# Kernel optimization log

Measured on AMD Instinct MI355X. Metric: run time of the kernel, lower is better.

Reference implementation:

```python
import jax, jax.numpy as jnp
import numpy as np

K = 3  # deformable kernel size
OFFSET_CLIP = 10.0


def _conv2d_same(x, w, b):
    # 3x3 conv, stride 1, padding 1, NCHW/OIHW
    out = jax.lax.conv_general_dilated(
        x, w, window_strides=(1, 1), padding=((1, 1), (1, 1)),
        dimension_numbers=("NCHW", "OIHW", "NCHW"))
    return out + b[None, :, None, None]


def _deform_conv2d(x, offset, weight):
    """torchvision-style deform_conv2d, stride 1, pad 1, dilation 1, no bias.
    x:      [B, C, H, W]
    offset: [B, 2*K*K, H, W]  (per tap: dy then dx)
    weight: [Cout, C, K, K]
    """
    B, C, H, W = x.shape
    off = offset.reshape(B, K * K, 2, H, W)
    ky, kx = jnp.meshgrid(jnp.arange(K, dtype=x.dtype), jnp.arange(K, dtype=x.dtype), indexing="ij")
    ky = ky.reshape(-1)  # [9]
    kx = kx.reshape(-1)
    # sample coords: p0 - pad + k + offset  -> [B, 9, H, W]
    ys = jnp.arange(H, dtype=x.dtype)[None, None, :, None] - 1.0 + ky[None, :, None, None] + off[:, :, 0]
    xs = jnp.arange(W, dtype=x.dtype)[None, None, None, :] - 1.0 + kx[None, :, None, None] + off[:, :, 1]
    y0 = jnp.floor(ys)
    x0 = jnp.floor(xs)
    ty = ys - y0  # fractional parts, [B,9,H,W]
    tx = xs - x0
    iy0 = y0.astype(jnp.int32)
    ix0 = x0.astype(jnp.int32)

    xf = x.reshape(B, C, H * W)

    def gather(iy, ix):
        valid = ((iy >= 0) & (iy < H) & (ix >= 0) & (ix < W)).astype(x.dtype)
        idx = (jnp.clip(iy, 0, H - 1) * W + jnp.clip(ix, 0, W - 1)).reshape(B, -1)
        v = jax.vmap(lambda xv, iv: xv[:, iv])(xf, idx)  # [B, C, 9*H*W]
        return v.reshape(B, C, K * K, H, W) * valid[:, None]

    v00 = gather(iy0, ix0)
    v01 = gather(iy0, ix0 + 1)
    v10 = gather(iy0 + 1, ix0)
    v11 = gather(iy0 + 1, ix0 + 1)

    w00 = ((1.0 - ty) * (1.0 - tx))[:, None]  # [B,1,9,H,W]
    w01 = ((1.0 - ty) * tx)[:, None]
    w10 = (ty * (1.0 - tx))[:, None]
    w11 = (ty * tx)[:, None]

    sampled = v00 * w00 + v01 * w01 + v10 * w10 + v11 * w11  # [B,C,9,H,W]
    return jnp.einsum("bckhw,ock->bohw", sampled, weight.reshape(weight.shape[0], C, K * K))


def setup_inputs() -> dict:
    key = jax.random.key(0)
    k1, k2, k3, k4 = jax.random.split(key, 4)
    B, C, H, W = 4, 64, 128, 128
    x = jax.random.normal(k1, (B, C, H, W), dtype=jnp.float32)
    ref = jax.random.normal(k2, (B, C, H, W), dtype=jnp.float32)
    # offset_conv: in=2C, out=2*3*3=18. (Original zero-inits; we use small random
    # weights so the deformable sampling path is nontrivially exercised.)
    offset_w = jax.random.normal(k3, (2 * K * K, 2 * C, K, K), dtype=jnp.float32) * 0.01
    offset_b = jnp.zeros((2 * K * K,), dtype=jnp.float32)
    # main deform weight: kaiming_normal fan_out, relu -> std = sqrt(2 / (Cout*K*K))
    std = float(np.sqrt(2.0 / (C * K * K)))
    weight = jax.random.normal(k4, (C, C, K, K), dtype=jnp.float32) * std
    return {"x": x, "ref": ref, "offset_w": offset_w, "offset_b": offset_b, "weight": weight}


def reference(x, ref, offset_w, offset_b, weight):
    combined = jnp.concatenate([x, ref], axis=1)
    offset = _conv2d_same(combined, offset_w, offset_b)
    offset = jnp.clip(offset, -OFFSET_CLIP, OFFSET_CLIP)
    aligned = _deform_conv2d(x, offset, weight)
    return aligned.astype(x.dtype)
```

## Files before the change

### kernel.cpp

```cpp
#include <hip/hip_runtime.h>

#define Bsz 4
#define Cch 64
#define Hh 128
#define Ww 128
#define NOFF 18
#define CK 576
#define CKPAD 580

typedef __attribute__((ext_vector_type(8))) short short8;
typedef __attribute__((ext_vector_type(4))) float floatx4;

__device__ __forceinline__ unsigned short f2bf(float f) {
    union { float f; unsigned u; } v; v.f = f;
    unsigned r = v.u + 0x7fff + ((v.u >> 16) & 1);
    return (unsigned short)(r >> 16);
}
__device__ __forceinline__ float bflo(unsigned d) {
    union { unsigned u; float f; } v; v.u = d << 16; return v.f;
}
__device__ __forceinline__ float bfhi(unsigned d) {
    union { unsigned u; float f; } v; v.u = d & 0xffff0000u; return v.f;
}
__device__ __forceinline__ unsigned cvtpk(float lo, float hi) {
    unsigned r;
    asm("v_cvt_pk_bf16_f32 %0, %1, %2" : "=v"(r) : "v"(lo), "v"(hi));
    return r;
}
__device__ __forceinline__ uint4 gld4(const void* p) {
    uint4 q;
    asm volatile("global_load_dwordx4 %0, %1, off" : "=v"(q) : "v"(p) : "memory");
    return q;
}

__global__ __launch_bounds__(256) void prep(const float* __restrict__ x,
                                            const float* __restrict__ ref,
                                            const float* __restrict__ wo,
                                            const float* __restrict__ w,
                                            unsigned* __restrict__ xpair,
                                            unsigned short* __restrict__ w9,
                                            unsigned short* __restrict__ wbf) {
    __shared__ unsigned tile[64][130];
    int bid = blockIdx.x;
    int tid = threadIdx.x;
    if (bid < 512) {
        int b = bid >> 7;
        int h = bid & 127;
        int px2 = tid & 63;
        int cg = tid >> 6;
        const float* xb = x + ((size_t)b << 20) + (h << 7) + (px2 << 1);
        const float* rb = ref + ((size_t)b << 20) + (h << 7) + (px2 << 1);
#pragma unroll
        for (int j = 0; j < 16; ++j) {
            int c0 = cg * 32 + 2 * j;
            const float* s = (c0 < 64) ? xb : rb;
            int cl = c0 & 63;
            float2 va = *(const float2*)(s + ((size_t)cl << 14));
            float2 vb = *(const float2*)(s + ((size_t)(cl + 1) << 14));
            unsigned w0 = (unsigned)f2bf(va.x) | ((unsigned)f2bf(vb.x) << 16);
            unsigned w1 = (unsigned)f2bf(va.y) | ((unsigned)f2bf(vb.y) << 16);
            *(uint2*)(&tile[c0 >> 1][px2 << 1]) = make_uint2(w0, w1);
        }
        __syncthreads();
#pragma unroll
        for (int it = 0; it < 16; ++it) {
            int idx = it * 256 + tid;
            int cq5 = idx & 31;
            int pos = idx >> 5;
            int posn = min(pos + 1, 127);
            unsigned t0 = tile[2 * cq5][pos], t0n = tile[2 * cq5][posn];
            unsigned t1 = tile[2 * cq5 + 1][pos], t1n = tile[2 * cq5 + 1][posn];
            uint4 o;
            o.x = (t0 & 0xffffu) | (t0n << 16);
            o.y = (t0 >> 16) | (t0n & 0xffff0000u);
            o.z = (t1 & 0xffffu) | (t1n << 16);
            o.w = (t1 >> 16) | (t1n & 0xffff0000u);
            *(uint4*)(xpair + (((size_t)(b << 14) + (h << 7) + pos) << 7) + (cq5 << 2)) = o;
        }
    } else if (bid < 656) {
        int t = (bid - 512) * 256 + tid;
        if (t < Cch * CK) {
            int oc = t / CK;
            int rem = t % CK;
            int k = rem >> 6, c = rem & 63;
            wbf[t] = f2bf(w[(oc * Cch + c) * 9 + k]);
        }
    } else {
        int t = (bid - 656) * 256 + tid;
        if (t < 9 * 32 * 128) {
            int ci = t & 127, ocp = (t >> 7) & 31, tap = t >> 12;
            w9[t] = (ocp < NOFF) ? f2bf(wo[(ocp * 128 + ci) * 9 + tap]) : (unsigned short)0;
        }
    }
}

__global__ __launch_bounds__(256, 3) void fused_align(
        const unsigned* __restrict__ xpair,
        const unsigned short* __restrict__ w9,
        const unsigned short* __restrict__ wbf,
        const float* __restrict__ bias,
        float* __restrict__ out) {
    __shared__ union {
        unsigned short tile3[3 * 34 * 128];
        unsigned short smp[32][CKPAD];
    } u;
    __shared__ float red[2][2][64][4];
    __shared__ float4 wts[288];
    __shared__ int2 meta[288];

    int bi0 = blockIdx.x;
    int bi = ((bi0 & 7) << 8) | (bi0 >> 3);
    int b = bi >> 9;
    int rem = bi & 511;
    int h = rem >> 2;
    int w0 = (rem & 3) << 5;
    int tid = threadIdx.x;
    int wv = tid >> 6, lane = tid & 63;
    int to = wv & 1;
    int kh = wv >> 1;
    int r16 = lane & 15;
    int g = lane >> 4;

    const unsigned* xp32 = xpair + ((size_t)b << 21);

    float bias4[4] = {0.f, 0.f, 0.f, 0.f};
    if (kh == 0) {
#pragma unroll
        for (int r = 0; r < 4; ++r) {
            int oc = to * 16 + g * 4 + r;
            if (oc < NOFF) bias4[r] = bias[oc];
        }
    }

    {
        uint4 qa[13];
        bool val[13];
#pragma unroll
        for (int it = 0; it < 13; ++it) {
            int idx = it * 256 + tid;
            int idc = (idx < 3264) ? idx : 0;
            int cq4 = idc & 31;
            int pos = idc >> 5;
            int row = pos / 34, xx = pos % 34;
            int yy = h + row - 1, xg = w0 + xx - 1;
            bool v = ((unsigned)yy < (unsigned)Hh) && ((unsigned)xg < (unsigned)Ww);
            val[it] = v;
            const unsigned* ap = xp32 + (((yy << 7) + xg) << 7) + (cq4 << 2);
            qa[it] = gld4(v ? (const void*)ap : (const void*)xp32);
        }
        asm volatile("s_waitcnt vmcnt(0)" ::: "memory");
        __builtin_amdgcn_sched_barrier(0);
#pragma unroll
        for (int it = 0; it < 13; ++it) {
            int idx = it * 256 + tid;
            if (idx < 3264) {
                int cq4 = idx & 31;
                int pos = idx >> 5;
                int xx = pos % 34;
                uint4 q = val[it] ? qa[it] : make_uint4(0u, 0u, 0u, 0u);
                unsigned p0v = (q.x & 0xffffu) | (q.y << 16);
                unsigned p1v = (q.z & 0xffffu) | (q.w << 16);
                int ci0 = cq4 << 2;
                *(uint2*)(&u.tile3[(pos << 7) + (ci0 ^ ((xx & 7) << 3))]) =
                    make_uint2(p0v, p1v);
            }
        }
    }
    __syncthreads();

    floatx4 accA0 = {0.f, 0.f, 0.f, 0.f};
    floatx4 accA1 = {0.f, 0.f, 0.f, 0.f};
#pragma unroll
    for (int tap = 0; tap < 9; ++tap) {
        int dy = tap / 3, dx = tap % 3;
        const unsigned short* arow = w9 + ((size_t)(tap * 32 + to * 16 + r16) << 7) + kh * 64;
        short8 a0 = *(const short8*)(arow + g * 8);
        short8 a1 = *(const short8*)(arow + 32 + g * 8);
#pragma unroll
        for (int s = 0; s < 2; ++s) {
            int xxr = r16 + dx + s * 16;
            const unsigned short* brow = &u.tile3[(dy * 34 + xxr) << 7];
            int sw = (xxr & 7) << 3;
            int cb0 = kh * 64 + g * 8;
            short8 bb0 = *(const short8*)(brow + (cb0 ^ sw));
            short8 bb1 = *(const short8*)(brow + ((cb0 + 32) ^ sw));
            if (s == 0) {
                accA0 = __builtin_amdgcn_mfma_f32_16x16x32_bf16(a0, bb0, accA0, 0, 0, 0);
                accA0 = __builtin_amdgcn_mfma_f32_16x16x32_bf16(a1, bb1, accA0, 0, 0, 0);
            } else {
                accA1 = __builtin_amdgcn_mfma_f32_16x16x32_bf16(a0, bb0, accA1, 0, 0, 0);
                accA1 = __builtin_amdgcn_mfma_f32_16x16x32_bf16(a1, bb1, accA1, 0, 0, 0);
            }
        }
    }
    if (kh == 1) {
#pragma unroll
        for (int r = 0; r < 4; ++r) { red[0][to][lane][r] = accA0[r]; red[1][to][lane][r] = accA1[r]; }
    }
    __syncthreads();

    if (kh == 0 && (to == 0 || g == 0)) {
        int ntap = (to == 0) ? 2 : 1;
        int kbase = (to * 16 + g * 4) >> 1;
#pragma unroll
        for (int s = 0; s < 2; ++s) {
            float vout[4];
#pragma unroll
            for (int r = 0; r < 4; ++r) {
                float v = (s == 0 ? accA0[r] : accA1[r]) + red[s][to][lane][r] + bias4[r];
                vout[r] = fminf(fmaxf(v, -10.0f), 10.0f);
            }
            int p = s * 16 + r16;
#pragma unroll
            for (int t = 0; t < 2; ++t) {
                if (t < ntap) {
                    int k = kbase + t;
                    float dyo = vout[2 * t], dxo = vout[2 * t + 1];
                    int ky = k / 3, kx = k % 3;
                    float ys = (float)(h - 1 + ky) + dyo;
                    float xs = (float)(w0 + p - 1 + kx) + dxo;
                    float fy = floorf(ys), fx = floorf(xs);
                    int iy0 = (int)fy, ix0 = (int)fx;
                    float ty = ys - fy, tx = xs - fx;
                    float wy0 = (1.f - ty) * (((unsigned)iy0 < (unsigned)Hh) ? 1.f : 0.f);
                    float wy1 = ty         * (((unsigned)(iy0 + 1) < (unsigned)Hh) ? 1.f : 0.f);
                    float wx0 = (1.f - tx) * (((unsigned)ix0 < (unsigned)Ww) ? 1.f : 0.f);
                    float wx1 = tx         * (((unsigned)(ix0 + 1) < (unsigned)Ww) ? 1.f : 0.f);
                    int ixb  = min(max(ix0, 0), Ww - 2);
                    int iy0c = min(max(iy0, 0), Hh - 1);
                    int iy1c = min(max(iy0 + 1, 0), Hh - 1);
                    bool s0v = (min(max(ix0, 0), Ww - 1) != ixb);
                    bool s1v = (min(max(ix0 + 1, 0), Ww - 1) != ixb);
                    float w00 = wy0 * wx0, w01 = wy0 * wx1, w10 = wy1 * wx0, w11 = wy1 * wx1;
                    float A  = (s0v ? 0.f : w00) + (s1v ? 0.f : w01);
                    float Bw = (s0v ? w00 : 0.f) + (s1v ? w01 : 0.f);
                    float Cw = (s0v ? 0.f : w10) + (s1v ? 0.f : w11);
                    float Dw = (s0v ? w10 : 0.f) + (s1v ? w11 : 0.f);
                    wts[p * 9 + k] = make_float4(A, Bw, Cw, Dw);
                    meta[p * 9 + k] = make_int2(((iy0c << 7) + ixb) << 9,
                                                ((iy1c << 7) + ixb) << 9);
                }
            }
        }
    }
    __syncthreads();

    {
        int p0 = tid >> 4, cq = tid & 15;
        const char* xbB = (const char*)xpair + ((size_t)b << 23) + cq * 16;
#pragma unroll
        for (int s = 0; s < 2; ++s) {
            int p = p0 + s * 16;
            uint4 q0[9], q1[9];
            float4 wt[9];
#pragma unroll
            for (int k = 0; k < 9; ++k) {
                int2 mm = meta[p * 9 + k];
                wt[k] = wts[p * 9 + k];
                q0[k] = gld4(xbB + mm.x);
                q1[k] = gld4(xbB + mm.y);
            }
            asm volatile("s_waitcnt vmcnt(0)" ::: "memory");
            __builtin_amdgcn_sched_barrier(0);
#pragma unroll
            for (int k = 0; k < 9; ++k) {
                uint4 qa = q0[k], qb = q1[k];
                float4 w = wt[k];
                float s0 = bflo(qa.x)*w.x + bfhi(qa.x)*w.y + bflo(qb.x)*w.z + bfhi(qb.x)*w.w;
                float s1 = bflo(qa.y)*w.x + bfhi(qa.y)*w.y + bflo(qb.y)*w.z + bfhi(qb.y)*w.w;
                float s2 = bflo(qa.z)*w.x + bfhi(qa.z)*w.y + bflo(qb.z)*w.z + bfhi(qb.z)*w.w;
                float s3 = bflo(qa.w)*w.x + bfhi(qa.w)*w.y + bflo(qb.w)*w.z + bfhi(qb.w)*w.w;
                *(uint2*)(&u.smp[p][k * 64 + cq * 4]) =
                    make_uint2(cvtpk(s0, s1), cvtpk(s2, s3));
            }
        }
    }
    __syncthreads();

    {
        floatx4 acc0 = {0.f, 0.f, 0.f, 0.f};
        floatx4 acc1 = {0.f, 0.f, 0.f, 0.f};
        const short8* ap = (const short8*)(wbf + (size_t)(wv * 16 + r16) * CK + g * 8);
        const unsigned short* bb0 = &u.smp[r16][g * 8];
        const unsigned short* bb1 = &u.smp[16 + r16][g * 8];
#pragma unroll
        for (int kk = 0; kk < 18; ++kk) {
            short8 a = ap[kk * 4];
            short8 v0 = *(const short8*)(bb0 + kk * 32);
            short8 v1 = *(const short8*)(bb1 + kk * 32);
            acc0 = __builtin_amdgcn_mfma_f32_16x16x32_bf16(a, v0, acc0, 0, 0, 0);
            acc1 = __builtin_amdgcn_mfma_f32_16x16x32_bf16(a, v1, acc1, 0, 0, 0);
        }
        size_t obase = ((size_t)(b * Cch + wv * 16 + g * 4)) << 14;
        int hw = (h << 7) + w0 + r16;
#pragma unroll
        for (int r = 0; r < 4; ++r) {
            out[obase + ((size_t)r << 14) + hw] = acc0[r];
            out[obase + ((size_t)r << 14) + hw + 16] = acc1[r];
        }
    }
}

extern "C" void kernel_launch(void* const* d_in, const int* in_sizes, int n_in,
                              void* d_out, int out_size, void* d_ws, size_t ws_size,
                              hipStream_t stream) {
    const float* x      = (const float*)d_in[0];
    const float* ref    = (const float*)d_in[1];
    const float* wo     = (const float*)d_in[2];
    const float* bias   = (const float*)d_in[3];
    const float* weight = (const float*)d_in[4];
    float* out = (float*)d_out;

    unsigned short* w9  = (unsigned short*)d_ws;
    unsigned short* wbf = (unsigned short*)((char*)d_ws + 262144);
    unsigned* xpair     = (unsigned*)((char*)d_ws + 524288);

    hipLaunchKernelGGL(prep, dim3(800), dim3(256), 0, stream,
                       x, ref, wo, weight, xpair, w9, wbf);
    hipLaunchKernelGGL(fused_align, dim3(2048), dim3(256), 0, stream,
                       xpair, w9, wbf, bias, out);
}
```

Measured before the change: 75.87 us.

## Overlap second-half gathers with first-half MFMA in deform conv

Splits the 32-pixel tile into two 16-pixel halves. It issues the bilinear gather loads for the second half before running the MFMA and output stores of the first half, so global gather latency overlaps with matrix compute. In exchange it adds a barrier, reloads the weight fragments for each half, and keeps 18 extra vector registers live across the MFMA loop, which may reduce occupancy.

```diff
diff --git a/kernel.cpp b/kernel.cpp
--- a/kernel.cpp
+++ b/kernel.cpp
@@ -248,56 +248,82 @@
     {
         int p0 = tid >> 4, cq = tid & 15;
         const char* xbB = (const char*)xpair + ((size_t)b << 23) + cq * 16;
-#pragma unroll
-        for (int s = 0; s < 2; ++s) {
-            int p = p0 + s * 16;
+        int p1 = p0 + 16;
+
+#define PACK9(p, qq0, qq1)                                                            \
+        _Pragma("unroll")                                                             \
+        for (int k = 0; k < 9; ++k) {                                                 \
+            float4 w = wts[(p) * 9 + k];                                              \
+            uint4 qa = qq0[k], qb = qq1[k];                                           \
+            float s0 = bflo(qa.x)*w.x + bfhi(qa.x)*w.y + bflo(qb.x)*w.z + bfhi(qb.x)*w.w; \
+            float s1 = bflo(qa.y)*w.x + bfhi(qa.y)*w.y + bflo(qb.y)*w.z + bfhi(qb.y)*w.w; \
+            float s2 = bflo(qa.z)*w.x + bfhi(qa.z)*w.y + bflo(qb.z)*w.z + bfhi(qb.z)*w.w; \
+            float s3 = bflo(qa.w)*w.x + bfhi(qa.w)*w.y + bflo(qb.w)*w.z + bfhi(qb.w)*w.w; \
+            *(uint2*)(&u.smp[p][k * 64 + cq * 4]) =                                   \
+                make_uint2(cvtpk(s0, s1), cvtpk(s2, s3));                             \
+        }
+
+        {
             uint4 q0[9], q1[9];
-            float4 wt[9];
 #pragma unroll
             for (int k = 0; k < 9; ++k) {
-                int2 mm = meta[p * 9 + k];
-                wt[k] = wts[p * 9 + k];
+                int2 mm = meta[p0 * 9 + k];
                 q0[k] = gld4(xbB + mm.x);
                 q1[k] = gld4(xbB + mm.y);
             }
             asm volatile("s_waitcnt vmcnt(0)" ::: "memory");
             __builtin_amdgcn_sched_barrier(0);
-#pragma unroll
-            for (int k = 0; k < 9; ++k) {
-                uint4 qa = q0[k], qb = q1[k];
-                float4 w = wt[k];
-                float s0 = bflo(qa.x)*w.x + bfhi(qa.x)*w.y + bflo(qb.x)*w.z + bfhi(qb.x)*w.w;
-                float s1 = bflo(qa.y)*w.x + bfhi(qa.y)*w.y + bflo(qb.y)*w.z + bfhi(qb.y)*w.w;
-                float s2 = bflo(qa.z)*w.x + bfhi(qa.z)*w.y + bflo(qb.z)*w.z + bfhi(qb.z)*w.w;
-                float s3 = bflo(qa.w)*w.x + bfhi(qa.w)*w.y + bflo(qb.w)*w.z + bfhi(qb.w)*w.w;
-                *(uint2*)(&u.smp[p][k * 64 + cq * 4]) =
-                    make_uint2(cvtpk(s0, s1), cvtpk(s2, s3));
-            }
-        }
-    }
-    __syncthreads();
-
-    {
-        floatx4 acc0 = {0.f, 0.f, 0.f, 0.f};
-        floatx4 acc1 = {0.f, 0.f, 0.f, 0.f};
-        const short8* ap = (const short8*)(wbf + (size_t)(wv * 16 + r16) * CK + g * 8);
-        const unsigned short* bb0 = &u.smp[r16][g * 8];
-        const unsigned short* bb1 = &u.smp[16 + r16][g * 8];
-#pragma unroll
-        for (int kk = 0; kk < 18; ++kk) {
-            short8 a = ap[kk * 4];
-            short8 v0 = *(const short8*)(bb0 + kk * 32);
-            short8 v1 = *(const short8*)(bb1 + kk * 32);
-            acc0 = __builtin_amdgcn_mfma_f32_16x16x32_bf16(a, v0, acc0, 0, 0, 0);
-            acc1 = __builtin_amdgcn_mfma_f32_16x16x32_bf16(a, v1, acc1, 0, 0, 0);
-        }
-        size_t obase = ((size_t)(b * Cch + wv * 16 + g * 4)) << 14;
-        int hw = (h << 7) + w0 + r16;
-#pragma unroll
-        for (int r = 0; r < 4; ++r) {
-            out[obase + ((size_t)r << 14) + hw] = acc0[r];
-            out[obase + ((size_t)r << 14) + hw + 16] = acc1[r];
-        }
+            PACK9(p0, q0, q1)
+        }
+
+        uint4 r0[9], r1[9];
+#pragma unroll
+        for (int k = 0; k < 9; ++k) {
+            int2 mm = meta[p1 * 9 + k];
+            r0[k] = gld4(xbB + mm.x);
+            r1[k] = gld4(xbB + mm.y);
+        }
+        __syncthreads();
+
+        {
+            floatx4 acc0 = {0.f, 0.f, 0.f, 0.f};
+            const short8* ap = (const short8*)(wbf + (size_t)(wv * 16 + r16) * CK + g * 8);
+            const unsigned short* bb0 = &u.smp[r16][g * 8];
+#pragma unroll
+            for (int kk = 0; kk < 18; ++kk) {
+                short8 a = ap[kk * 4];
+                short8 v0 = *(const short8*)(bb0 + kk * 32);
+                acc0 = __builtin_amdgcn_mfma_f32_16x16x32_bf16(a, v0, acc0, 0, 0, 0);
+            }
+            size_t obase = ((size_t)(b * Cch + wv * 16 + g * 4)) << 14;
+            int hw = (h << 7) + w0 + r16;
+#pragma unroll
+            for (int r = 0; r < 4; ++r)
+                out[obase + ((size_t)r << 14) + hw] = acc0[r];
+        }
+
+        asm volatile("s_waitcnt vmcnt(0)" ::: "memory");
+        __builtin_amdgcn_sched_barrier(0);
+        PACK9(p1, r0, r1)
+        __syncthreads();
+
+        {
+            floatx4 acc1 = {0.f, 0.f, 0.f, 0.f};
+            const short8* ap = (const short8*)(wbf + (size_t)(wv * 16 + r16) * CK + g * 8);
+            const unsigned short* bb1 = &u.smp[16 + r16][g * 8];
+#pragma unroll
+            for (int kk = 0; kk < 18; ++kk) {
+                short8 a = ap[kk * 4];
+                short8 v1 = *(const short8*)(bb1 + kk * 32);
+                acc1 = __builtin_amdgcn_mfma_f32_16x16x32_bf16(a, v1, acc1, 0, 0, 0);
+            }
+            size_t obase = ((size_t)(b * Cch + wv * 16 + g * 4)) << 14;
+            int hw = (h << 7) + w0 + r16 + 16;
+#pragma unroll
+            for (int r = 0; r < 4; ++r)
+                out[obase + ((size_t)r << 14) + hw] = acc1[r];
+        }
+#undef PACK9
     }
 }
 
```

Result: slower. 82.13 us (+8.3%).

## Shrink LDS footprint to fit four blocks per CU via union overlap

Applied to the files above, without the earlier changes.

Moves the reduction buffer, sampling weights and metadata into the same LDS union as the sampled tile, stores bilinear weights as packed fp16 instead of float4, and replaces the padded sampled-matrix layout with an XOR-swizzled unpadded one. Because the metadata now overlaps the sample buffer, the second pixel pass first copies its metadata into registers and adds extra barriers before overwriting. The aim is to cut LDS per block so launch bounds can request four blocks per CU, hiding gather latency with more waves. It risks register pressure under the tighter bound, extra syncs, and fp16 rounding of the interpolation weights.

```diff
diff --git a/kernel.cpp b/kernel.cpp
--- a/kernel.cpp
+++ b/kernel.cpp
@@ -6,10 +6,11 @@
 #define Ww 128
 #define NOFF 18
 #define CK 576
-#define CKPAD 580
+#define SMPB 1152
 
 typedef __attribute__((ext_vector_type(8))) short short8;
 typedef __attribute__((ext_vector_type(4))) float floatx4;
+typedef __fp16 half2v __attribute__((ext_vector_type(2)));
 
 __device__ __forceinline__ unsigned short f2bf(float f) {
     union { float f; unsigned u; } v; v.f = f;
@@ -27,10 +28,19 @@
     asm("v_cvt_pk_bf16_f32 %0, %1, %2" : "=v"(r) : "v"(lo), "v"(hi));
     return r;
 }
+__device__ __forceinline__ unsigned h2bits(half2v h) {
+    union { half2v h; unsigned u; } v; v.h = h; return v.u;
+}
+__device__ __forceinline__ half2v bits2h(unsigned u) {
+    union { half2v h; unsigned u; } v; v.u = u; return v.h;
+}
 __device__ __forceinline__ uint4 gld4(const void* p) {
     uint4 q;
     asm volatile("global_load_dwordx4 %0, %1, off" : "=v"(q) : "v"(p) : "memory");
     return q;
+}
+__device__ __forceinline__ char* smpp(char* base, int row, int bir) {
+    return base + row * SMPB + (bir ^ ((row & 7) << 4));
 }
 
 __global__ __launch_bounds__(256) void prep(const float* __restrict__ x,
@@ -94,19 +104,21 @@
     }
 }
 
-__global__ __launch_bounds__(256, 3) void fused_align(
+__global__ __launch_bounds__(256, 4) void fused_align(
         const unsigned* __restrict__ xpair,
         const unsigned short* __restrict__ w9,
         const unsigned short* __restrict__ wbf,
         const float* __restrict__ bias,
         float* __restrict__ out) {
     __shared__ union {
-        unsigned short tile3[3 * 34 * 128];
-        unsigned short smp[32][CKPAD];
+        struct {
+            unsigned short tile3[3 * 34 * 128];
+            float red[2][2][64][4];
+            uint2 wtsH[288];
+            int2 metaB[288];
+        } A;
+        unsigned short smp[32][576];
     } u;
-    __shared__ float red[2][2][64][4];
-    __shared__ float4 wts[288];
-    __shared__ int2 meta[288];
 
     int bi0 = blockIdx.x;
     int bi = ((bi0 & 7) << 8) | (bi0 >> 3);
@@ -161,7 +173,7 @@
                 unsigned p0v = (q.x & 0xffffu) | (q.y << 16);
                 unsigned p1v = (q.z & 0xffffu) | (q.w << 16);
                 int ci0 = cq4 << 2;
-                *(uint2*)(&u.tile3[(pos << 7) + (ci0 ^ ((xx & 7) << 3))]) =
+                *(uint2*)(&u.A.tile3[(pos << 7) + (ci0 ^ ((xx & 7) << 3))]) =
                     make_uint2(p0v, p1v);
             }
         }
@@ -179,7 +191,7 @@
 #pragma unroll
         for (int s = 0; s < 2; ++s) {
             int xxr = r16 + dx + s * 16;
-            const unsigned short* brow = &u.tile3[(dy * 34 + xxr) << 7];
+            const unsigned short* brow = &u.A.tile3[(dy * 34 + xxr) << 7];
             int sw = (xxr & 7) << 3;
             int cb0 = kh * 64 + g * 8;
             short8 bb0 = *(const short8*)(brow + (cb0 ^ sw));
@@ -195,7 +207,7 @@
     }
     if (kh == 1) {
 #pragma unroll
-        for (int r = 0; r < 4; ++r) { red[0][to][lane][r] = accA0[r]; red[1][to][lane][r] = accA1[r]; }
+        for (int r = 0; r < 4; ++r) { u.A.red[0][to][lane][r] = accA0[r]; u.A.red[1][to][lane][r] = accA1[r]; }
     }
     __syncthreads();
 
@@ -207,7 +219,7 @@
             float vout[4];
 #pragma unroll
             for (int r = 0; r < 4; ++r) {
-                float v = (s == 0 ? accA0[r] : accA1[r]) + red[s][to][lane][r] + bias4[r];
+                float v = (s == 0 ? accA0[r] : accA1[r]) + u.A.red[s][to][lane][r] + bias4[r];
                 vout[r] = fminf(fmaxf(v, -10.0f), 10.0f);
             }
             int p = s * 16 + r16;
@@ -236,9 +248,11 @@
                     float Bw = (s0v ? w00 : 0.f) + (s1v ? w01 : 0.f);
                     float Cw = (s0v ? 0.f : w10) + (s1v ? 0.f : w11);
                     float Dw = (s0v ? w10 : 0.f) + (s1v ? w11 : 0.f);
-                    wts[p * 9 + k] = make_float4(A, Bw, Cw, Dw);
-                    meta[p * 9 + k] = make_int2(((iy0c << 7) + ixb) << 9,
-                                                ((iy1c << 7) + ixb) << 9);
+                    u.A.wtsH[p * 9 + k] = make_uint2(
+                        h2bits(__builtin_amdgcn_cvt_pkrtz(A, Bw)),
+                        h2bits(__builtin_amdgcn_cvt_pkrtz(Cw, Dw)));
+                    u.A.metaB[p * 9 + k] = make_int2(((iy0c << 7) + ixb) << 9,
+                                                     ((iy1c << 7) + ixb) << 9);
                 }
             }
         }
@@ -248,15 +262,26 @@
     {
         int p0 = tid >> 4, cq = tid & 15;
         const char* xbB = (const char*)xpair + ((size_t)b << 23) + cq * 16;
-#pragma unroll
-        for (int s = 0; s < 2; ++s) {
-            int p = p0 + s * 16;
+        char* smpBase = (char*)u.smp;
+
+#define PACK1(p, qa, qb, whx, why)                                                    \
+        {                                                                             \
+            half2v hAB = bits2h(whx), hCD = bits2h(why);                              \
+            float wAv = (float)hAB.x, wBv = (float)hAB.y;                             \
+            float wCv = (float)hCD.x, wDv = (float)hCD.y;                             \
+            float s0 = bflo(qa.x)*wAv + bfhi(qa.x)*wBv + bflo(qb.x)*wCv + bfhi(qb.x)*wDv; \
+            float s1 = bflo(qa.y)*wAv + bfhi(qa.y)*wBv + bflo(qb.y)*wCv + bfhi(qb.y)*wDv; \
+            float s2 = bflo(qa.z)*wAv + bfhi(qa.z)*wBv + bflo(qb.z)*wCv + bfhi(qb.z)*wDv; \
+            float s3 = bflo(qa.w)*wAv + bfhi(qa.w)*wBv + bflo(qb.w)*wCv + bfhi(qb.w)*wDv; \
+            *(uint2*)smpp(smpBase, p, k * 128 + cq * 8) =                             \
+                make_uint2(cvtpk(s0, s1), cvtpk(s2, s3));                             \
+        }
+
+        {
             uint4 q0[9], q1[9];
-            float4 wt[9];
-#pragma unroll
-            for (int k = 0; k < 9; ++k) {
-                int2 mm = meta[p * 9 + k];
-                wt[k] = wts[p * 9 + k];
+#pragma unroll
+            for (int k = 0; k < 9; ++k) {
+                int2 mm = u.A.metaB[p0 * 9 + k];
                 q0[k] = gld4(xbB + mm.x);
                 q1[k] = gld4(xbB + mm.y);
             }
@@ -265,29 +290,50 @@
 #pragma unroll
             for (int k = 0; k < 9; ++k) {
                 uint4 qa = q0[k], qb = q1[k];
-                float4 w = wt[k];
-                float s0 = bflo(qa.x)*w.x + bfhi(qa.x)*w.y + bflo(qb.x)*w.z + bfhi(qb.x)*w.w;
-                float s1 = bflo(qa.y)*w.x + bfhi(qa.y)*w.y + bflo(qb.y)*w.z + bfhi(qb.y)*w.w;
-                float s2 = bflo(qa.z)*w.x + bfhi(qa.z)*w.y + bflo(qb.z)*w.z + bfhi(qb.z)*w.w;
-                float s3 = bflo(qa.w)*w.x + bfhi(qa.w)*w.y + bflo(qb.w)*w.z + bfhi(qb.w)*w.w;
-                *(uint2*)(&u.smp[p][k * 64 + cq * 4]) =
-                    make_uint2(cvtpk(s0, s1), cvtpk(s2, s3));
-            }
-        }
+                uint2 wh = u.A.wtsH[p0 * 9 + k];
+                PACK1(p0, qa, qb, wh.x, wh.y)
+            }
+        }
+        __syncthreads();
+
+        {
+            int p1 = p0 + 16;
+            int2 mreg[9];
+            uint2 wreg[9];
+#pragma unroll
+            for (int k = 0; k < 9; ++k) {
+                mreg[k] = u.A.metaB[p1 * 9 + k];
+                wreg[k] = u.A.wtsH[p1 * 9 + k];
+            }
+            __syncthreads();
+            uint4 q0[9], q1[9];
+#pragma unroll
+            for (int k = 0; k < 9; ++k) {
+                q0[k] = gld4(xbB + mreg[k].x);
+                q1[k] = gld4(xbB + mreg[k].y);
+            }
+            asm volatile("s_waitcnt vmcnt(0)" ::: "memory");
+            __builtin_amdgcn_sched_barrier(0);
+#pragma unroll
+            for (int k = 0; k < 9; ++k) {
+                uint4 qa = q0[k], qb = q1[k];
+                PACK1(p1, qa, qb, wreg[k].x, wreg[k].y)
+            }
+        }
+#undef PACK1
     }
     __syncthreads();
 
     {
+        char* smpBase = (char*)u.smp;
         floatx4 acc0 = {0.f, 0.f, 0.f, 0.f};
         floatx4 acc1 = {0.f, 0.f, 0.f, 0.f};
         const short8* ap = (const short8*)(wbf + (size_t)(wv * 16 + r16) * CK + g * 8);
-        const unsigned short* bb0 = &u.smp[r16][g * 8];
-        const unsigned short* bb1 = &u.smp[16 + r16][g * 8];
 #pragma unroll
         for (int kk = 0; kk < 18; ++kk) {
             short8 a = ap[kk * 4];
-            short8 v0 = *(const short8*)(bb0 + kk * 32);
-            short8 v1 = *(const short8*)(bb1 + kk * 32);
+            short8 v0 = *(const short8*)smpp(smpBase, r16, g * 16 + kk * 64);
+            short8 v1 = *(const short8*)smpp(smpBase, 16 + r16, g * 16 + kk * 64);
             acc0 = __builtin_amdgcn_mfma_f32_16x16x32_bf16(a, v0, acc0, 0, 0, 0);
             acc1 = __builtin_amdgcn_mfma_f32_16x16x32_bf16(a, v1, acc1, 0, 0, 0);
         }
```

Measured after the change: 66.63 us (median of 2 runs). -12.2%, faster.

## Shrink LDS footprint to raise occupancy: union buffers, fp16 weights, half-size sample tile

Applied to the files above, without the earlier changes.

Moves the reduction buffer into the shared union with the input tile, stores bilinear weights as packed fp16, and halves the sampled tile to 16 pixels. Sampling and the MFMA GEMM now alternate per 16-pixel half, with an XOR swizzle on the sample buffer. This cuts LDS use so the launch bound can rise from 3 to 5 blocks per SIMD, aiming to hide gather latency. In exchange it adds extra barriers, serialises the two halves, and loses some precision from fp16 weights.

```diff
diff --git a/kernel.cpp b/kernel.cpp
--- a/kernel.cpp
+++ b/kernel.cpp
@@ -6,10 +6,11 @@
 #define Ww 128
 #define NOFF 18
 #define CK 576
-#define CKPAD 580
+#define SMPB 1152
 
 typedef __attribute__((ext_vector_type(8))) short short8;
 typedef __attribute__((ext_vector_type(4))) float floatx4;
+typedef __fp16 half2v __attribute__((ext_vector_type(2)));
 
 __device__ __forceinline__ unsigned short f2bf(float f) {
     union { float f; unsigned u; } v; v.f = f;
@@ -27,10 +28,19 @@
     asm("v_cvt_pk_bf16_f32 %0, %1, %2" : "=v"(r) : "v"(lo), "v"(hi));
     return r;
 }
+__device__ __forceinline__ unsigned h2bits(half2v h) {
+    union { half2v h; unsigned u; } v; v.h = h; return v.u;
+}
+__device__ __forceinline__ half2v bits2h(unsigned u) {
+    union { half2v h; unsigned u; } v; v.u = u; return v.h;
+}
 __device__ __forceinline__ uint4 gld4(const void* p) {
     uint4 q;
     asm volatile("global_load_dwordx4 %0, %1, off" : "=v"(q) : "v"(p) : "memory");
     return q;
+}
+__device__ __forceinline__ char* smpp(char* base, int row, int bir) {
+    return base + row * SMPB + (bir ^ ((row & 7) << 4));
 }
 
 __global__ __launch_bounds__(256) void prep(const float* __restrict__ x,
@@ -94,19 +104,23 @@
     }
 }
 
-__global__ __launch_bounds__(256, 3) void fused_align(
+__global__ __launch_bounds__(256, 5) void fused_align(
         const unsigned* __restrict__ xpair,
         const unsigned short* __restrict__ w9,
         const unsigned short* __restrict__ wbf,
         const float* __restrict__ bias,
         float* __restrict__ out) {
     __shared__ union {
-        unsigned short tile3[3 * 34 * 128];
-        unsigned short smp[32][CKPAD];
+        struct {
+            unsigned short tile3[3 * 34 * 128];
+            float red[2][2][64][4];
+        } A;
+        struct {
+            uint2 wtsH[288];
+            int2 metaB[288];
+            unsigned short smp[16][576];
+        } B;
     } u;
-    __shared__ float red[2][2][64][4];
-    __shared__ float4 wts[288];
-    __shared__ int2 meta[288];
 
     int bi0 = blockIdx.x;
     int bi = ((bi0 & 7) << 8) | (bi0 >> 3);
@@ -161,7 +175,7 @@
                 unsigned p0v = (q.x & 0xffffu) | (q.y << 16);
                 unsigned p1v = (q.z & 0xffffu) | (q.w << 16);
                 int ci0 = cq4 << 2;
-                *(uint2*)(&u.tile3[(pos << 7) + (ci0 ^ ((xx & 7) << 3))]) =
+                *(uint2*)(&u.A.tile3[(pos << 7) + (ci0 ^ ((xx & 7) << 3))]) =
                     make_uint2(p0v, p1v);
             }
         }
@@ -179,7 +193,7 @@
 #pragma unroll
         for (int s = 0; s < 2; ++s) {
             int xxr = r16 + dx + s * 16;
-            const unsigned short* brow = &u.tile3[(dy * 34 + xxr) << 7];
+            const unsigned short* brow = &u.A.tile3[(dy * 34 + xxr) << 7];
             int sw = (xxr & 7) << 3;
             int cb0 = kh * 64 + g * 8;
             short8 bb0 = *(const short8*)(brow + (cb0 ^ sw));
@@ -195,7 +209,7 @@
     }
     if (kh == 1) {
 #pragma unroll
-        for (int r = 0; r < 4; ++r) { red[0][to][lane][r] = accA0[r]; red[1][to][lane][r] = accA1[r]; }
+        for (int r = 0; r < 4; ++r) { u.A.red[0][to][lane][r] = accA0[r]; u.A.red[1][to][lane][r] = accA1[r]; }
     }
     __syncthreads();
 
@@ -207,7 +221,7 @@
             float vout[4];
 #pragma unroll
             for (int r = 0; r < 4; ++r) {
-                float v = (s == 0 ? accA0[r] : accA1[r]) + red[s][to][lane][r] + bias4[r];
+                float v = (s == 0 ? accA0[r] : accA1[r]) + u.A.red[s][to][lane][r] + bias4[r];
                 vout[r] = fminf(fmaxf(v, -10.0f), 10.0f);
             }
             int p = s * 16 + r16;
@@ -236,9 +250,11 @@
                     float Bw = (s0v ? w00 : 0.f) + (s1v ? w01 : 0.f);
                     float Cw = (s0v ? 0.f : w10) + (s1v ? 0.f : w11);
                     float Dw = (s0v ? w10 : 0.f) + (s1v ? w11 : 0.f);
-                    wts[p * 9 + k] = make_float4(A, Bw, Cw, Dw);
-                    meta[p * 9 + k] = make_int2(((iy0c << 7) + ixb) << 9,
-                                                ((iy1c << 7) + ixb) << 9);
+                    u.B.wtsH[p * 9 + k] = make_uint2(
+                        h2bits(__builtin_amdgcn_cvt_pkrtz(A, Bw)),
+                        h2bits(__builtin_amdgcn_cvt_pkrtz(Cw, Dw)));
+                    u.B.metaB[p * 9 + k] = make_int2(((iy0c << 7) + ixb) << 9,
+                                                     ((iy1c << 7) + ixb) << 9);
                 }
             }
         }
@@ -248,55 +264,55 @@
     {
         int p0 = tid >> 4, cq = tid & 15;
         const char* xbB = (const char*)xpair + ((size_t)b << 23) + cq * 16;
+        char* smpBase = (char*)u.B.smp;
+        size_t obase = ((size_t)(b * Cch + wv * 16 + g * 4)) << 14;
+        int hwb = (h << 7) + w0 + r16;
+
 #pragma unroll
         for (int s = 0; s < 2; ++s) {
             int p = p0 + s * 16;
-            uint4 q0[9], q1[9];
-            float4 wt[9];
-#pragma unroll
-            for (int k = 0; k < 9; ++k) {
-                int2 mm = meta[p * 9 + k];
-                wt[k] = wts[p * 9 + k];
-                q0[k] = gld4(xbB + mm.x);
-                q1[k] = gld4(xbB + mm.y);
-            }
-            asm volatile("s_waitcnt vmcnt(0)" ::: "memory");
-            __builtin_amdgcn_sched_barrier(0);
-#pragma unroll
-            for (int k = 0; k < 9; ++k) {
-                uint4 qa = q0[k], qb = q1[k];
-                float4 w = wt[k];
-                float s0 = bflo(qa.x)*w.x + bfhi(qa.x)*w.y + bflo(qb.x)*w.z + bfhi(qb.x)*w.w;
-                float s1 = bflo(qa.y)*w.x + bfhi(qa.y)*w.y + bflo(qb.y)*w.z + bfhi(qb.y)*w.w;
-                float s2 = bflo(qa.z)*w.x + bfhi(qa.z)*w.y + bflo(qb.z)*w.z + bfhi(qb.z)*w.w;
-                float s3 = bflo(qa.w)*w.x + bfhi(qa.w)*w.y + bflo(qb.w)*w.z + bfhi(qb.w)*w.w;
-                *(uint2*)(&u.smp[p][k * 64 + cq * 4]) =
-                    make_uint2(cvtpk(s0, s1), cvtpk(s2, s3));
-            }
-        }
-    }
-    __syncthreads();
-
-    {
-        floatx4 acc0 = {0.f, 0.f, 0.f, 0.f};
-        floatx4 acc1 = {0.f, 0.f, 0.f, 0.f};
-        const short8* ap = (const short8*)(wbf + (size_t)(wv * 16 + r16) * CK + g * 8);
-        const unsigned short* bb0 = &u.smp[r16][g * 8];
-        const unsigned short* bb1 = &u.smp[16 + r16][g * 8];
-#pragma unroll
-        for (int kk = 0; kk < 18; ++kk) {
-            short8 a = ap[kk * 4];
-            short8 v0 = *(const short8*)(bb0 + kk * 32);
-            short8 v1 = *(const short8*)(bb1 + kk * 32);
-            acc0 = __builtin_amdgcn_mfma_f32_16x16x32_bf16(a, v0, acc0, 0, 0, 0);
-            acc1 = __builtin_amdgcn_mfma_f32_16x16x32_bf16(a, v1, acc1, 0, 0, 0);
-        }
-        size_t obase = ((size_t)(b * Cch + wv * 16 + g * 4)) << 14;
-        int hw = (h << 7) + w0 + r16;
-#pragma unroll
-        for (int r = 0; r < 4; ++r) {
-            out[obase + ((size_t)r << 14) + hw] = acc0[r];
-            out[obase + ((size_t)r << 14) + hw + 16] = acc1[r];
+            {
+                uint4 q0[9], q1[9];
+#pragma unroll
+                for (int k = 0; k < 9; ++k) {
+                    int2 mm = u.B.metaB[p * 9 + k];
+                    q0[k] = gld4(xbB + mm.x);
+                    q1[k] = gld4(xbB + mm.y);
+                }
+                asm volatile("s_waitcnt vmcnt(0)" ::: "memory");
+                __builtin_amdgcn_sched_barrier(0);
+#pragma unroll
+                for (int k = 0; k < 9; ++k) {
+                    uint2 wh = u.B.wtsH[p * 9 + k];
+                    half2v hAB = bits2h(wh.x), hCD = bits2h(wh.y);
+                    float wAv = (float)hAB.x, wBv = (float)hAB.y;
+                    float wCv = (float)hCD.x, wDv = (float)hCD.y;
+                    uint4 qa = q0[k], qb = q1[k];
+                    float s0 = bflo(qa.x)*wAv + bfhi(qa.x)*wBv + bflo(qb.x)*wCv + bfhi(qb.x)*wDv;
+                    float s1 = bflo(qa.y)*wAv + bfhi(qa.y)*wBv + bflo(qb.y)*wCv + bfhi(qb.y)*wDv;
+                    float s2 = bflo(qa.z)*wAv + bfhi(qa.z)*wBv + bflo(qb.z)*wCv + bfhi(qb.z)*wDv;
+                    float s3 = bflo(qa.w)*wAv + bfhi(qa.w)*wBv + bflo(qb.w)*wCv + bfhi(qb.w)*wDv;
+                    *(uint2*)smpp(smpBase, p0, k * 128 + cq * 8) =
+                        make_uint2(cvtpk(s0, s1), cvtpk(s2, s3));
+                }
+            }
+            __syncthreads();
+
+            {
+                floatx4 acc = {0.f, 0.f, 0.f, 0.f};
+                const short8* ap = (const short8*)(wbf + (size_t)(wv * 16 + r16) * CK + g * 8);
+#pragma unroll
+                for (int kk = 0; kk < 18; ++kk) {
+                    short8 a = ap[kk * 4];
+                    short8 v0 = *(const short8*)smpp(smpBase, r16, g * 16 + kk * 64);
+                    acc = __builtin_amdgcn_mfma_f32_16x16x32_bf16(a, v0, acc, 0, 0, 0);
+                }
+                int hw = hwb + s * 16;
+#pragma unroll
+                for (int r = 0; r < 4; ++r)
+                    out[obase + ((size_t)r << 14) + hw] = acc[r];
+            }
+            if (s == 0) __syncthreads();
         }
     }
 }
```

New measurement: 86.47 us. +14.0%, slower.
